# Optimization experiments

Hardware: AMD Instinct MI355X
Metric: run time of the kernel (lower is better)

The kernel has to match this reference:

```python
import jax, jax.numpy as jnp
import numpy as np

B, NU, NI, E, FU, FI = 128, 10000, 10000, 64, 8, 8
IN = 2 * E + FU + FI  # GRUCell input size = 144
EPS = 1e-12


def _gru_cell(x, h, w_ih, w_hh, b_ih, b_hh):
    # torch.nn.GRUCell math; here h == 0 (cell is called without a hidden state).
    gi = x @ w_ih.T + b_ih            # (B, 3E)
    gh = h @ w_hh.T + b_hh            # (B, 3E)
    i_r, i_z, i_n = jnp.split(gi, 3, axis=-1)
    h_r, h_z, h_n = jnp.split(gh, 3, axis=-1)
    r = jax.nn.sigmoid(i_r + h_r)
    z = jax.nn.sigmoid(i_z + h_z)
    n = jnp.tanh(i_n + r * h_n)
    return (1.0 - z) * n + z * h


def _l2_normalize(x):
    # torch F.normalize(dim=1): x / max(||x||_2, eps)
    nrm = jnp.sqrt(jnp.sum(x * x, axis=1, keepdims=True))
    return x / jnp.maximum(nrm, EPS)


def setup_inputs() -> dict:
    key = jax.random.key(0)
    ks = jax.random.split(key, 14)
    s = 1.0 / np.sqrt(E)  # torch GRUCell default init scale
    return {
        "user_memory": jax.random.normal(ks[0], (B, NU, E), jnp.float32),
        "item_memory": jax.random.normal(ks[1], (B, NI, E), jnp.float32),
        "user_ids": jax.random.randint(ks[2], (B,), 0, NU),
        "item_ids": jax.random.randint(ks[3], (B,), 0, NI),
        "user_features": jax.random.normal(ks[4], (B, FU), jnp.float32),
        "item_features": jax.random.normal(ks[5], (B, FI), jnp.float32),
        "u_w_ih": jax.random.uniform(ks[6], (3 * E, IN), jnp.float32, -s, s),
        "u_w_hh": jax.random.uniform(ks[7], (3 * E, E), jnp.float32, -s, s),
        "u_b_ih": jax.random.uniform(ks[8], (3 * E,), jnp.float32, -s, s),
        "u_b_hh": jax.random.uniform(ks[9], (3 * E,), jnp.float32, -s, s),
        "i_w_ih": jax.random.uniform(ks[10], (3 * E, IN), jnp.float32, -s, s),
        "i_w_hh": jax.random.uniform(ks[11], (3 * E, E), jnp.float32, -s, s),
        "i_b_ih": jax.random.uniform(ks[12], (3 * E,), jnp.float32, -s, s),
        "i_b_hh": jax.random.uniform(ks[13], (3 * E,), jnp.float32, -s, s),
    }


def reference(user_memory, item_memory, user_ids, item_ids, user_features,
              item_features, u_w_ih, u_w_hh, u_b_ih, u_b_hh,
              i_w_ih, i_w_hh, i_b_ih, i_b_hh):
    b = jnp.arange(user_ids.shape[0])
    user_emb = user_memory[b, user_ids, :]   # gather (B, E)
    item_emb = item_memory[b, item_ids, :]   # gather (B, E)
    user_in = jnp.concatenate([user_emb, user_features, item_emb, item_features], axis=1)
    item_in = jnp.concatenate([item_emb, item_features, user_emb, user_features], axis=1)
    h0 = jnp.zeros_like(user_emb)
    new_user = _l2_normalize(_gru_cell(user_in, h0, u_w_ih, u_w_hh, u_b_ih, u_b_hh))
    new_item = _l2_normalize(_gru_cell(item_in, h0, i_w_ih, i_w_hh, i_b_ih, i_b_hh))
    new_user_memory = user_memory.at[b, user_ids, :].set(new_user)  # scatter back
    new_item_memory = item_memory.at[b, item_ids, :].set(new_item)
    return new_user, new_item, new_user_memory, new_item_memory
```

## Files before the change

### kernel.cpp

```cpp
#include <hip/hip_runtime.h>
#include <math.h>

#define BATCH   128
#define NUSER   10000
#define NITEM   10000
#define EDIM    64
#define FUDIM   8
#define FIDIM   8
#define INDIM   144

typedef float v4f __attribute__((ext_vector_type(4)));

#define OFF_NI   ((long)BATCH * EDIM)
#define OFF_UM   ((long)2 * BATCH * EDIM)
#define MEM_ELTS ((long)BATCH * NUSER * EDIM)
#define OFF_IM   (OFF_UM + MEM_ELTS)

__global__ __launch_bounds__(64) void limnet_gru_kernel(
    const float* __restrict__ um, const float* __restrict__ im,
    const int* __restrict__ uids, const int* __restrict__ iids,
    const float* __restrict__ ufeat, const float* __restrict__ ifeat,
    const float* __restrict__ u_w_ih, const float* __restrict__ u_b_ih,
    const float* __restrict__ u_b_hh,
    const float* __restrict__ i_w_ih, const float* __restrict__ i_b_ih,
    const float* __restrict__ i_b_hh,
    float* __restrict__ out)
{
    const int unit  = blockIdx.x;
    const int b     = unit >> 1;
    const int which = unit & 1;
    const int lane  = threadIdx.x;

    __shared__ float x[INDIM];

    const int uid = uids[b];
    const int iid = iids[b];
    const float* ue = um + ((long)b * NUSER + uid) * EDIM;
    const float* ie = im + ((long)b * NITEM + iid) * EDIM;

    if (which == 0) {
        x[lane] = ue[lane];
        x[EDIM + FUDIM + lane] = ie[lane];
        if (lane < FUDIM) x[EDIM + lane] = ufeat[b * FUDIM + lane];
        if (lane < FIDIM) x[EDIM + FUDIM + EDIM + lane] = ifeat[b * FIDIM + lane];
    } else {
        x[lane] = ie[lane];
        x[EDIM + FIDIM + lane] = ue[lane];
        if (lane < FIDIM) x[EDIM + lane] = ifeat[b * FIDIM + lane];
        if (lane < FUDIM) x[EDIM + FIDIM + EDIM + lane] = ufeat[b * FUDIM + lane];
    }
    __syncthreads();

    const float* w   = which ? i_w_ih : u_w_ih;
    const float* bih = which ? i_b_ih : u_b_ih;
    const float* bhh = which ? i_b_hh : u_b_hh;

    float gr = bih[lane];
    float gz = bih[EDIM + lane];
    float gn = bih[2 * EDIM + lane];
    const v4f* wr = (const v4f*)(w + (long)lane * INDIM);
    const v4f* wz = (const v4f*)(w + (long)(EDIM + lane) * INDIM);
    const v4f* wn = (const v4f*)(w + (long)(2 * EDIM + lane) * INDIM);
    #pragma unroll 6
    for (int k4 = 0; k4 < INDIM / 4; ++k4) {
        const v4f vr = wr[k4];
        const v4f vz = wz[k4];
        const v4f vn = wn[k4];
        const float x0 = x[4 * k4 + 0], x1 = x[4 * k4 + 1];
        const float x2 = x[4 * k4 + 2], x3 = x[4 * k4 + 3];
        gr = fmaf(vr.x, x0, gr); gr = fmaf(vr.y, x1, gr);
        gr = fmaf(vr.z, x2, gr); gr = fmaf(vr.w, x3, gr);
        gz = fmaf(vz.x, x0, gz); gz = fmaf(vz.y, x1, gz);
        gz = fmaf(vz.z, x2, gz); gz = fmaf(vz.w, x3, gz);
        gn = fmaf(vn.x, x0, gn); gn = fmaf(vn.y, x1, gn);
        gn = fmaf(vn.z, x2, gn); gn = fmaf(vn.w, x3, gn);
    }
    const float r = 1.0f / (1.0f + expf(-(gr + bhh[lane])));
    const float z = 1.0f / (1.0f + expf(-(gz + bhh[EDIM + lane])));
    const float n = tanhf(gn + r * bhh[2 * EDIM + lane]);
    const float h = (1.0f - z) * n;

    float s = h * h;
    #pragma unroll
    for (int off = 32; off; off >>= 1) s += __shfl_xor(s, off, 64);
    const float val = h / fmaxf(sqrtf(s), 1e-12f);

    if (which == 0) {
        out[(long)b * EDIM + lane] = val;
        out[OFF_UM + ((long)b * NUSER + uid) * EDIM + lane] = val;
    } else {
        out[OFF_NI + (long)b * EDIM + lane] = val;
        out[OFF_IM + ((long)b * NITEM + iid) * EDIM + lane] = val;
    }
}

extern "C" void kernel_launch(void* const* d_in, const int* in_sizes, int n_in,
                              void* d_out, int out_size, void* d_ws, size_t ws_size,
                              hipStream_t stream) {
    const float* um    = (const float*)d_in[0];
    const float* im    = (const float*)d_in[1];
    const int*   uids  = (const int*)d_in[2];
    const int*   iids  = (const int*)d_in[3];
    const float* ufeat = (const float*)d_in[4];
    const float* ifeat = (const float*)d_in[5];
    const float* u_w_ih = (const float*)d_in[6];
    const float* u_b_ih = (const float*)d_in[8];
    const float* u_b_hh = (const float*)d_in[9];
    const float* i_w_ih = (const float*)d_in[10];
    const float* i_b_ih = (const float*)d_in[12];
    const float* i_b_hh = (const float*)d_in[13];
    float* out = (float*)d_out;

    const size_t mem_bytes = (size_t)MEM_ELTS * sizeof(float);
    hipMemcpyAsync(out + OFF_UM, um, mem_bytes, hipMemcpyDeviceToDevice, stream);
    hipMemcpyAsync(out + OFF_IM, im, mem_bytes, hipMemcpyDeviceToDevice, stream);

    limnet_gru_kernel<<<BATCH * 2, 64, 0, stream>>>(
        um, im, uids, iids, ufeat, ifeat,
        u_w_ih, u_b_ih, u_b_hh,
        i_w_ih, i_b_ih, i_b_hh,
        out);
}
```

Measured before the change: 260.6 us.

## Fuse memory-table copy into GRU kernel with nontemporal vector copies

Replaces two device-to-device memcpys and a separate GRU launch with one kernel whose leading blocks copy both memory tables using nontemporal 16-byte loads/stores, skipping the rows that the GRU blocks later scatter to. Trailing blocks run the GRU with four units per 256-thread block. This removes launch/serialization overhead and avoids redundant writes of scattered rows, at the cost of per-thread index math and an id lookup in the copy path.

Result: faster. 250.6 us (-3.8%).

```diff
diff --git a/kernel.cpp b/kernel.cpp
--- a/kernel.cpp
+++ b/kernel.cpp
@@ -15,8 +15,10 @@
 #define OFF_UM   ((long)2 * BATCH * EDIM)
 #define MEM_ELTS ((long)BATCH * NUSER * EDIM)
 #define OFF_IM   (OFF_UM + MEM_ELTS)
+#define NBLK_PER_MEM ((int)(MEM_ELTS / 4 / 256))
+#define GRU_BLOCKS   64
 
-__global__ __launch_bounds__(64) void limnet_gru_kernel(
+__global__ __launch_bounds__(256) void limnet_fused_kernel(
     const float* __restrict__ um, const float* __restrict__ im,
     const int* __restrict__ uids, const int* __restrict__ iids,
     const float* __restrict__ ufeat, const float* __restrict__ ifeat,
@@ -26,12 +28,34 @@
     const float* __restrict__ i_b_hh,
     float* __restrict__ out)
 {
-    const int unit  = blockIdx.x;
+    const int blk = blockIdx.x;
+
+    if (blk < 2 * NBLK_PER_MEM) {
+        const bool isU = blk < NBLK_PER_MEM;
+        const int  lblk = isU ? blk : blk - NBLK_PER_MEM;
+        const v4f* __restrict__ src = isU ? (const v4f*)um : (const v4f*)im;
+        v4f* __restrict__ dst = isU ? (v4f*)(out + OFF_UM) : (v4f*)(out + OFF_IM);
+        const int* __restrict__ ids = isU ? uids : iids;
+
+        const long i   = (long)lblk * 256 + threadIdx.x;
+        const int  row = (int)(i >> 4);
+        const int  b   = row / NUSER;
+        const int  idx = row - b * NUSER;
+
+        const v4f val = __builtin_nontemporal_load(&src[i]);
+        if (idx != ids[b])
+            __builtin_nontemporal_store(val, &dst[i]);
+        return;
+    }
+
+    const int unit  = (blk - 2 * NBLK_PER_MEM) * 4 + (threadIdx.x >> 6);
     const int b     = unit >> 1;
     const int which = unit & 1;
-    const int lane  = threadIdx.x;
+    const int lane  = threadIdx.x & 63;
+    const int wv    = threadIdx.x >> 6;
 
-    __shared__ float x[INDIM];
+    __shared__ float xs[4][INDIM];
+    float* x = xs[wv];
 
     const int uid = uids[b];
     const int iid = iids[b];
@@ -61,7 +85,7 @@
     const v4f* wr = (const v4f*)(w + (long)lane * INDIM);
     const v4f* wz = (const v4f*)(w + (long)(EDIM + lane) * INDIM);
     const v4f* wn = (const v4f*)(w + (long)(2 * EDIM + lane) * INDIM);
-    #pragma unroll 6
+    #pragma unroll 4
     for (int k4 = 0; k4 < INDIM / 4; ++k4) {
         const v4f vr = wr[k4];
         const v4f vz = wz[k4];
@@ -111,11 +135,7 @@
     const float* i_b_hh = (const float*)d_in[13];
     float* out = (float*)d_out;
 
-    const size_t mem_bytes = (size_t)MEM_ELTS * sizeof(float);
-    hipMemcpyAsync(out + OFF_UM, um, mem_bytes, hipMemcpyDeviceToDevice, stream);
-    hipMemcpyAsync(out + OFF_IM, im, mem_bytes, hipMemcpyDeviceToDevice, stream);
-
-    limnet_gru_kernel<<<BATCH * 2, 64, 0, stream>>>(
+    limnet_fused_kernel<<<2 * NBLK_PER_MEM + GRU_BLOCKS, 256, 0, stream>>>(
         um, im, uids, iids, ufeat, ifeat,
         u_w_ih, u_b_ih, u_b_hh,
         i_w_ih, i_b_ih, i_b_hh,
```
